# Performance work log

Measured on AMD Instinct MI355X. Metric: run time of the kernel, lower is better.

Reference implementation:

```python
import jax, jax.numpy as jnp
import numpy as np

B, C, O, H, W = 4, 256, 256, 64, 64
KH = KW = 3
KK = KH * KW
PAD = 1  # stride=1, padding=1 -> output spatial == input spatial


def setup_inputs() -> dict:
    key = jax.random.key(0)
    k0, k1, k2, k3 = jax.random.split(key, 4)
    x = jax.random.normal(k0, (B, C, H, W), jnp.float32)
    # offset-predicting conv: small weights -> realistic sub-pixel offsets
    w_off = jax.random.normal(k1, (3 * KK, C, KH, KW), jnp.float32) * 0.01
    b_off = jnp.zeros((3 * KK,), jnp.float32)
    w_def = jax.random.normal(k2, (O, C, KH, KW), jnp.float32) * (1.0 / np.sqrt(C * KK))
    b_def = jax.random.normal(k3, (O,), jnp.float32) * 0.01
    return {"x": x, "w_off": w_off, "b_off": b_off, "w_def": w_def, "b_def": b_def}


def _conv2d(x, w, b):
    y = jax.lax.conv_general_dilated(
        x, w, window_strides=(1, 1), padding=((PAD, PAD), (PAD, PAD)),
        dimension_numbers=("NCHW", "OIHW", "NCHW"))
    return y + b[None, :, None, None]


def _deform_conv2d(x, offsets, mask, w, b):
    # torchvision modulated DeformConv2d, stride=1, pad=1, dilation=1.
    Bx, Cx, Hx, Wx = x.shape
    Ox = w.shape[0]
    # offsets: [B, 2*KK, H, W] with channel 2k = dy, 2k+1 = dx for tap k
    off = offsets.reshape(Bx, KK, 2, Hx, Wx)
    ky, kx = jnp.meshgrid(jnp.arange(KH), jnp.arange(KW), indexing="ij")
    ky = ky.reshape(KK)
    kx = kx.reshape(KK)
    base_y = (ky[:, None, None] - PAD + jnp.arange(Hx)[None, :, None]).astype(x.dtype)  # [KK,H,1]
    base_x = (kx[:, None, None] - PAD + jnp.arange(Wx)[None, None, :]).astype(x.dtype)  # [KK,1,W]
    sy = off[:, :, 0] + base_y  # [B,KK,H,W] sample rows
    sx = off[:, :, 1] + base_x  # [B,KK,H,W] sample cols

    y0 = jnp.floor(sy)
    x0 = jnp.floor(sx)
    ty = sy - y0  # fractional weights (grad flows to offsets through these)
    tx = sx - x0

    x_flat = x.reshape(Bx, Cx, Hx * Wx)
    val = jnp.zeros((Bx, Cx, KK, Hx, Wx), x.dtype)
    for dy in (0, 1):  # 4 bilinear corners (fixed small loop)
        for dx in (0, 1):
            yi = y0.astype(jnp.int32) + dy
            xi = x0.astype(jnp.int32) + dx
            wgt = (ty if dy else 1.0 - ty) * (tx if dx else 1.0 - tx)
            valid = (yi >= 0) & (yi < Hx) & (xi >= 0) & (xi < Wx)  # zero outside
            idx = (jnp.clip(yi, 0, Hx - 1) * Wx + jnp.clip(xi, 0, Wx - 1)).reshape(Bx, 1, -1)
            g = jnp.take_along_axis(x_flat, idx, axis=2).reshape(Bx, Cx, KK, Hx, Wx)
            val = val + g * jnp.where(valid, wgt, 0.0)[:, None]

    val = val * mask.reshape(Bx, 1, KK, Hx, Wx)  # modulation
    out = jnp.einsum("bckhw,ock->bohw", val, w.reshape(Ox, Cx, KK))
    return out + b[None, :, None, None]


def reference(x, w_off, b_off, w_def, b_def):
    pred = _conv2d(x, w_off, b_off)            # [B, 3*KK, H, W]
    offsets = pred[:, : 2 * KK]                # [B, 2*KK, H, W]
    mask = jax.nn.sigmoid(pred[:, 2 * KK:])    # [B, KK, H, W]
    return _deform_conv2d(x, offsets, mask, w_def, b_def)
```

## Files before the change

kernel.cpp:

```cpp
#include <hip/hip_runtime.h>

#define BB 4
#define CCH 256
#define OCH 256
#define HH 64
#define WW 64
#define HWSZ 4096

typedef __bf16 bf16_t;
typedef bf16_t bf16x8 __attribute__((ext_vector_type(8)));
typedef bf16_t bf16x2_t __attribute__((ext_vector_type(2)));
typedef float f32x4 __attribute__((ext_vector_type(4)));

__device__ __forceinline__ unsigned int packbf(float a, float b) {
    bf16x2_t p;
    p.x = (__bf16)a;
    p.y = (__bf16)b;
    return __builtin_bit_cast(unsigned int, p);
}
__device__ __forceinline__ float blo(unsigned int u) { return __uint_as_float(u << 16); }
__device__ __forceinline__ float bhi(unsigned int u) { return __uint_as_float(u & 0xFFFF0000u); }

__device__ __forceinline__ void block_sync() {
    asm volatile("s_waitcnt lgkmcnt(0)" ::: "memory");
    __builtin_amdgcn_s_barrier();
    __builtin_amdgcn_sched_barrier(0);
}

__global__ __launch_bounds__(256) void k_prep(const float* __restrict__ x,
                                              const float* __restrict__ w_off,
                                              const float* __restrict__ w_def,
                                              ushort* __restrict__ xT,
                                              ushort* __restrict__ w1F,
                                              ushort* __restrict__ w2F,
                                              float* __restrict__ P) {
    int bid = blockIdx.x;
    if (bid < 256) {
        int b = bid >> 6;
        int h = bid & 63;
        int tid = threadIdx.x;
        int wv = tid >> 6;
        int lane = tid & 63;

        __shared__ unsigned int buf[64][130];

        const float* xp = x + ((size_t)b * CCH + wv * 64) * HWSZ + h * WW + lane;
#pragma unroll 8
        for (int i = 0; i < 32; ++i) {
            float a = xp[(size_t)(2 * i) * HWSZ];
            float c = xp[(size_t)(2 * i + 1) * HWSZ];
            buf[lane][wv * 32 + i] = packbf(a, c);
        }
        __syncthreads();

        ushort* dst = xT + ((size_t)(b * 64 + h) * 64) * 256;
#pragma unroll
        for (int r = 0; r < 16; ++r) {
            int idx = tid + r * 256;
            int w = idx >> 6;
            int q = idx & 63;
            uint2 v = *(const uint2*)&buf[w][2 * q];
            *(uint2*)(dst + (size_t)w * 256 + q * 4) = v;
        }
        return;
    }

    int i = (bid - 256) * 256 + threadIdx.x;
    if (i < 73728) {
        int j = i & 7;
        int o = (i >> 3) & 31;
        int cSub = (i >> 8) & 31;
        int k = i >> 13;
        float v = 0.0f;
        if (o < 27) v = w_off[((size_t)o * CCH + cSub * 8 + j) * 9 + k];
        w1F[i] = (ushort)(packbf(v, 0.f) & 0xFFFFu);
        return;
    }
    i -= 73728;
    if (i < 589824) {
        int j = i & 7;
        int o = (i >> 3) & 255;
        int cg = (i >> 11) & 31;
        int k = i >> 16;
        float v = w_def[(size_t)o * 2304 + (cg * 8 + j) * 9 + k];
        w2F[i] = (ushort)(packbf(v, 0.f) & 0xFFFFu);
        return;
    }
    i -= 589824;
    if (i < 110592) {
        ((float4*)P)[i] = make_float4(0.f, 0.f, 0.f, 0.f);
    }
}

__global__ __launch_bounds__(512) void k_pred4(const ushort* __restrict__ xT,
                                               const ushort* __restrict__ w1F,
                                               float* __restrict__ P) {
    int bid = blockIdx.x;
    int L = (bid & 7) * 64 + (bid >> 3);
    int cs = L & 3;
    int hg = (L >> 2) & 31;
    int b  = L >> 7;
    int tid = threadIdx.x;
    int lane = tid & 63;
    int wv   = tid >> 6;
    int l16  = lane & 15;
    int lq   = lane >> 4;
    int spx  = tid >> 3;
    int cl   = tid & 7;

    __shared__ ushort b_lds[2][8][8][16][8];

    const ushort* xTb = xT + (size_t)b * HWSZ * 256 + cs * 64 + cl * 8;
    const bf16x8* w1v = (const bf16x8*)w1F;

    f32x4 acc[2];
    acc[0] = (f32x4){0.f, 0.f, 0.f, 0.f};
    acc[1] = (f32x4){0.f, 0.f, 0.f, 0.f};

    auto stageLoad = [&](int k, int tpx) -> uint4 {
        int row = hg * 2 + (tpx >> 6);
        int col = tpx & 63;
        int ys = row + k / 3 - 1;
        int xs = col + k % 3 - 1;
        bool ok = (ys >= 0 && ys < HH && xs >= 0 && xs < WW);
        uint4 v = make_uint4(0u, 0u, 0u, 0u);
        if (ok) v = *(const uint4*)(xTb + (size_t)(ys * WW + xs) * 256);
        return v;
    };
    auto stageWrite = [&](uint4 v, int buf, int tpx) {
        *(uint4*)&b_lds[buf][cl][tpx >> 4][(tpx & 15) ^ cl][0] = v;
    };

    {
        uint4 v0 = stageLoad(0, spx);
        uint4 v1 = stageLoad(0, spx + 64);
        stageWrite(v0, 0, spx);
        stageWrite(v1, 0, spx + 64);
    }
    __syncthreads();

    for (int t = 0; t < 9; ++t) {
        int cur = t & 1;
        uint4 n0, n1;
        if (t < 8) {
            n0 = stageLoad(t + 1, spx);
            n1 = stageLoad(t + 1, spx + 64);
        }
        bf16x8 a00 = w1v[(size_t)(t * 32 + cs * 8 + 0 * 4 + lq) * 32 + 0 * 16 + l16];
        bf16x8 a01 = w1v[(size_t)(t * 32 + cs * 8 + 0 * 4 + lq) * 32 + 1 * 16 + l16];
        bf16x8 a10 = w1v[(size_t)(t * 32 + cs * 8 + 1 * 4 + lq) * 32 + 0 * 16 + l16];
        bf16x8 a11 = w1v[(size_t)(t * 32 + cs * 8 + 1 * 4 + lq) * 32 + 1 * 16 + l16];
        bf16x8 b0 = *(const bf16x8*)&b_lds[cur][0 * 4 + lq][wv][l16 ^ (0 * 4 + lq)][0];
        bf16x8 b1 = *(const bf16x8*)&b_lds[cur][1 * 4 + lq][wv][l16 ^ (1 * 4 + lq)][0];
        acc[0] = __builtin_amdgcn_mfma_f32_16x16x32_bf16(a00, b0, acc[0], 0, 0, 0);
        acc[1] = __builtin_amdgcn_mfma_f32_16x16x32_bf16(a01, b0, acc[1], 0, 0, 0);
        acc[0] = __builtin_amdgcn_mfma_f32_16x16x32_bf16(a10, b1, acc[0], 0, 0, 0);
        acc[1] = __builtin_amdgcn_mfma_f32_16x16x32_bf16(a11, b1, acc[1], 0, 0, 0);
        if (t < 8) {
            stageWrite(n0, cur ^ 1, spx);
            stageWrite(n1, cur ^ 1, spx + 64);
        }
        __syncthreads();
    }

    int prow = hg * 2 + (wv >> 2);
    int pcol = (wv & 3) * 16 + l16;
#pragma unroll
    for (int mf = 0; mf < 2; ++mf) {
#pragma unroll
        for (int r = 0; r < 4; ++r) {
            int o = mf * 16 + lq * 4 + r;
            if (o < 27) {
                atomicAdd(&P[((size_t)b * 27 + o) * HWSZ + prow * WW + pcol],
                          acc[mf][r]);
            }
        }
    }
}

__global__ __launch_bounds__(512, 4) void k_deform15(const ushort* __restrict__ xT,
                                                     const float* __restrict__ P,
                                                     const float* __restrict__ b_off,
                                                     const ushort* __restrict__ w2F,
                                                     const float* __restrict__ b_def,
                                                     float* __restrict__ out) {
    int bid = blockIdx.x;
    int L = (bid & 7) * 64 + (bid >> 3);
    int ph = L & 1;
    int h  = (L >> 1) & 63;
    int b  = L >> 7;
    int px0 = ph * 32;
    int tid = threadIdx.x;
    int lane = tid & 63;
    int wv   = tid >> 6;
    int l16  = lane & 15;
    int lq   = lane >> 4;
    int pxs  = tid >> 4;
    int cl   = tid & 15;

    __shared__ ushort b_lds[2][16][2][16][8];

    const char* xTc = (const char*)xT + (size_t)b * HWSZ * 512 + cl * 16;
    const bf16x8* w2b = (const bf16x8*)w2F + wv * 32 + l16;

    uint4* wdst0 = (uint4*)&b_lds[0][cl][pxs >> 4][(pxs & 15) ^ cl][0];
    uint4* wdst1 = (uint4*)&b_lds[1][cl][pxs >> 4][(pxs & 15) ^ cl][0];

    f32x4 acc[2][2];
#pragma unroll
    for (int mf = 0; mf < 2; ++mf)
#pragma unroll
        for (int nt = 0; nt < 2; ++nt) acc[mf][nt] = (f32x4){0.f, 0.f, 0.f, 0.f};

    const float* Pb = P + (size_t)b * 27 * HWSZ + h * WW + px0 + pxs;

    float pOy, pOx, pMr, bOy, bOx, bMr;
    float wgt[4];
    const char* aptr[4];

    auto loadP = [&](int k) {
        pOy = Pb[(size_t)(2 * k) * HWSZ];
        pOx = Pb[(size_t)(2 * k + 1) * HWSZ];
        pMr = Pb[(size_t)(18 + k) * HWSZ];
        bOy = b_off[2 * k];
        bOx = b_off[2 * k + 1];
        bMr = b_off[18 + k];
    };
    auto calcDesc = [&](int k) {
        float offy = pOy + bOy;
        float offx = pOx + bOx;
        float m = 1.0f / (1.0f + expf(-(pMr + bMr)));
        float sy = offy + (float)(h + k / 3 - 1);
        float sx = offx + (float)(px0 + pxs + k % 3 - 1);
        float y0f = floorf(sy), x0f = floorf(sx);
        float ty = sy - y0f, tx = sx - x0f;
        int y0 = (int)y0f, x0 = (int)x0f;
#pragma unroll
        for (int dy = 0; dy < 2; ++dy) {
#pragma unroll
            for (int dx = 0; dx < 2; ++dx) {
                int yi = y0 + dy, xi = x0 + dx;
                bool ok = (yi >= 0 && yi < HH && xi >= 0 && xi < WW);
                float wg = (dy ? ty : 1.0f - ty) * (dx ? tx : 1.0f - tx) * m;
                wgt[dy * 2 + dx]  = ok ? wg : 0.0f;
                aptr[dy * 2 + dx] = xTc + (size_t)(ok ? (yi * WW + xi) : 0) * 512;
            }
        }
    };

    uint4 gbA[4], gbB[4];
    float wgtA[4], wgtB[4];
    bf16x8 aA[2][4], aB[2][4];

    auto issueGatherTo = [&](uint4 (&gb)[4], float (&wg)[4], int off) {
#pragma unroll
        for (int c = 0; c < 4; ++c) gb[c] = *(const uint4*)(aptr[c] + off);
#pragma unroll
        for (int c = 0; c < 4; ++c) wg[c] = wgt[c];
    };
    auto combineFrom = [&](const uint4 (&g)[4], const float (&w)[4]) -> uint4 {
        uint4 r;
        {
            float lo = w[0]*blo(g[0].x) + w[1]*blo(g[1].x) + w[2]*blo(g[2].x) + w[3]*blo(g[3].x);
            float hi = w[0]*bhi(g[0].x) + w[1]*bhi(g[1].x) + w[2]*bhi(g[2].x) + w[3]*bhi(g[3].x);
            r.x = packbf(lo, hi);
        }
        {
            float lo = w[0]*blo(g[0].y) + w[1]*blo(g[1].y) + w[2]*blo(g[2].y) + w[3]*blo(g[3].y);
            float hi = w[0]*bhi(g[0].y) + w[1]*bhi(g[1].y) + w[2]*bhi(g[2].y) + w[3]*bhi(g[3].y);
            r.y = packbf(lo, hi);
        }
        {
            float lo = w[0]*blo(g[0].z) + w[1]*blo(g[1].z) + w[2]*blo(g[2].z) + w[3]*blo(g[3].z);
            float hi = w[0]*bhi(g[0].z) + w[1]*bhi(g[1].z) + w[2]*bhi(g[2].z) + w[3]*bhi(g[3].z);
            r.z = packbf(lo, hi);
        }
        {
            float lo = w[0]*blo(g[0].w) + w[1]*blo(g[1].w) + w[2]*blo(g[2].w) + w[3]*blo(g[3].w);
            float hi = w[0]*bhi(g[0].w) + w[1]*bhi(g[1].w) + w[2]*bhi(g[2].w) + w[3]*bhi(g[3].w);
            r.w = packbf(lo, hi);
        }
        return r;
    };
    auto loadATo = [&](bf16x8 (&a)[2][4], int t) {
        size_t base = ((size_t)((t >> 1) * 32 + (t & 1) * 16) + lq) * 256;
#pragma unroll
        for (int g = 0; g < 4; ++g)
#pragma unroll
            for (int mf = 0; mf < 2; ++mf)
                a[mf][g] = w2b[base + (size_t)g * 1024 + mf * 16];
    };

#define MFMA_BODY(BUF, AREG)                                                        \
    do {                                                                            \
        bf16x8 bfr[4][2];                                                           \
        _Pragma("unroll")                                                           \
        for (int g = 0; g < 4; ++g) {                                               \
            int kg = g * 4 + lq;                                                    \
            _Pragma("unroll")                                                       \
            for (int nt = 0; nt < 2; ++nt)                                          \
                bfr[g][nt] = *(const bf16x8*)&b_lds[BUF][kg][nt][l16 ^ kg][0];      \
        }                                                                           \
        _Pragma("unroll")                                                           \
        for (int g = 0; g < 4; ++g)                                                 \
            _Pragma("unroll")                                                       \
            for (int mf = 0; mf < 2; ++mf)                                          \
                _Pragma("unroll")                                                   \
                for (int nt = 0; nt < 2; ++nt)                                      \
                    acc[mf][nt] = __builtin_amdgcn_mfma_f32_16x16x32_bf16(          \
                        AREG[mf][g], bfr[g][nt], acc[mf][nt], 0, 0, 0);             \
    } while (0)

    loadP(0);
    calcDesc(0);
    issueGatherTo(gbA, wgtA, 0);
    issueGatherTo(gbB, wgtB, 256);
    loadP(1);
    loadATo(aA, 0);
    *wdst0 = combineFrom(gbA, wgtA);
    __syncthreads();

    for (int tp = 0; tp < 9; ++tp) {
        if (tp < 8) {
            calcDesc(tp + 1);
            issueGatherTo(gbA, wgtA, 0);
        }
        loadATo(aB, 2 * tp + 1);
        MFMA_BODY(0, aA);
        *wdst1 = combineFrom(gbB, wgtB);
        __syncthreads();

        if (tp < 8) {
            issueGatherTo(gbB, wgtB, 256);
            if (tp < 7) loadP(tp + 2);
            loadATo(aA, 2 * tp + 2);
        }
        MFMA_BODY(1, aB);
        if (tp < 8) {
            *wdst0 = combineFrom(gbA, wgtA);
        }
        __syncthreads();
    }
#undef MFMA_BODY

#pragma unroll
    for (int mf = 0; mf < 2; ++mf) {
#pragma unroll
        for (int nt = 0; nt < 2; ++nt) {
#pragma unroll
            for (int r = 0; r < 4; ++r) {
                int o = wv * 32 + mf * 16 + lq * 4 + r;
                out[((size_t)b * OCH + o) * HWSZ + h * WW + px0 + nt * 16 + l16] =
                    acc[mf][nt][r] + b_def[o];
            }
        }
    }
}

extern "C" void kernel_launch(void* const* d_in, const int* in_sizes, int n_in,
                              void* d_out, int out_size, void* d_ws, size_t ws_size,
                              hipStream_t stream) {
    const float* x     = (const float*)d_in[0];
    const float* w_off = (const float*)d_in[1];
    const float* b_off = (const float*)d_in[2];
    const float* w_def = (const float*)d_in[3];
    const float* b_def = (const float*)d_in[4];
    float* out = (float*)d_out;

    float*  P   = (float*)d_ws;
    ushort* w1F = (ushort*)(P + (size_t)BB * 27 * HWSZ);
    ushort* w2F = w1F + 73728;
    ushort* xT  = w2F + 589824;

    hipLaunchKernelGGL(k_prep, dim3(3280), dim3(256), 0, stream,
                       x, w_off, w_def, xT, w1F, w2F, P);
    hipLaunchKernelGGL(k_pred4, dim3(512), dim3(512), 0, stream, xT, w1F, P);
    hipLaunchKernelGGL(k_deform15, dim3(512), dim3(512), 0, stream,
                       xT, P, b_off, w2F, b_def, out);
}
```

Before: 76.58 us.

## Restructure deform pipeline to process whole tap per stage with double-buffered LDS

```diff
diff --git a/kernel.cpp b/kernel.cpp
--- a/kernel.cpp
+++ b/kernel.cpp
@@ -20,12 +20,6 @@
 }
 __device__ __forceinline__ float blo(unsigned int u) { return __uint_as_float(u << 16); }
 __device__ __forceinline__ float bhi(unsigned int u) { return __uint_as_float(u & 0xFFFF0000u); }
-
-__device__ __forceinline__ void block_sync() {
-    asm volatile("s_waitcnt lgkmcnt(0)" ::: "memory");
-    __builtin_amdgcn_s_barrier();
-    __builtin_amdgcn_sched_barrier(0);
-}
 
 __global__ __launch_bounds__(256) void k_prep(const float* __restrict__ x,
                                               const float* __restrict__ w_off,
@@ -178,7 +172,7 @@
     }
 }
 
-__global__ __launch_bounds__(512, 4) void k_deform15(const ushort* __restrict__ xT,
+__global__ __launch_bounds__(512, 4) void k_deform16(const ushort* __restrict__ xT,
                                                      const float* __restrict__ P,
                                                      const float* __restrict__ b_off,
                                                      const ushort* __restrict__ w2F,
@@ -198,13 +192,15 @@
     int pxs  = tid >> 4;
     int cl   = tid & 15;
 
-    __shared__ ushort b_lds[2][16][2][16][8];
+    __shared__ ushort b_lds[2][2][16][2][16][8];
 
     const char* xTc = (const char*)xT + (size_t)b * HWSZ * 512 + cl * 16;
     const bf16x8* w2b = (const bf16x8*)w2F + wv * 32 + l16;
 
-    uint4* wdst0 = (uint4*)&b_lds[0][cl][pxs >> 4][(pxs & 15) ^ cl][0];
-    uint4* wdst1 = (uint4*)&b_lds[1][cl][pxs >> 4][(pxs & 15) ^ cl][0];
+    uint4* wdst00 = (uint4*)&b_lds[0][0][cl][pxs >> 4][(pxs & 15) ^ cl][0];
+    uint4* wdst01 = (uint4*)&b_lds[0][1][cl][pxs >> 4][(pxs & 15) ^ cl][0];
+    uint4* wdst10 = (uint4*)&b_lds[1][0][cl][pxs >> 4][(pxs & 15) ^ cl][0];
+    uint4* wdst11 = (uint4*)&b_lds[1][1][cl][pxs >> 4][(pxs & 15) ^ cl][0];
 
     f32x4 acc[2][2];
 #pragma unroll
@@ -249,41 +245,38 @@
     };
 
     uint4 gbA[4], gbB[4];
-    float wgtA[4], wgtB[4];
     bf16x8 aA[2][4], aB[2][4];
 
-    auto issueGatherTo = [&](uint4 (&gb)[4], float (&wg)[4], int off) {
+    auto issueGatherTo = [&](uint4 (&gb)[4], int off) {
 #pragma unroll
         for (int c = 0; c < 4; ++c) gb[c] = *(const uint4*)(aptr[c] + off);
-#pragma unroll
-        for (int c = 0; c < 4; ++c) wg[c] = wgt[c];
-    };
-    auto combineFrom = [&](const uint4 (&g)[4], const float (&w)[4]) -> uint4 {
+    };
+    auto combineFrom = [&](const uint4 (&g)[4]) -> uint4 {
         uint4 r;
         {
-            float lo = w[0]*blo(g[0].x) + w[1]*blo(g[1].x) + w[2]*blo(g[2].x) + w[3]*blo(g[3].x);
-            float hi = w[0]*bhi(g[0].x) + w[1]*bhi(g[1].x) + w[2]*bhi(g[2].x) + w[3]*bhi(g[3].x);
+            float lo = wgt[0]*blo(g[0].x) + wgt[1]*blo(g[1].x) + wgt[2]*blo(g[2].x) + wgt[3]*blo(g[3].x);
+            float hi = wgt[0]*bhi(g[0].x) + wgt[1]*bhi(g[1].x) + wgt[2]*bhi(g[2].x) + wgt[3]*bhi(g[3].x);
             r.x = packbf(lo, hi);
         }
         {
-            float lo = w[0]*blo(g[0].y) + w[1]*blo(g[1].y) + w[2]*blo(g[2].y) + w[3]*blo(g[3].y);
-            float hi = w[0]*bhi(g[0].y) + w[1]*bhi(g[1].y) + w[2]*bhi(g[2].y) + w[3]*bhi(g[3].y);
+            float lo = wgt[0]*blo(g[0].y) + wgt[1]*blo(g[1].y) + wgt[2]*blo(g[2].y) + wgt[3]*blo(g[3].y);
+            float hi = wgt[0]*bhi(g[0].y) + wgt[1]*bhi(g[1].y) + wgt[2]*bhi(g[2].y) + wgt[3]*bhi(g[3].y);
             r.y = packbf(lo, hi);
         }
         {
-            float lo = w[0]*blo(g[0].z) + w[1]*blo(g[1].z) + w[2]*blo(g[2].z) + w[3]*blo(g[3].z);
-            float hi = w[0]*bhi(g[0].z) + w[1]*bhi(g[1].z) + w[2]*bhi(g[2].z) + w[3]*bhi(g[3].z);
+            float lo = wgt[0]*blo(g[0].z) + wgt[1]*blo(g[1].z) + wgt[2]*blo(g[2].z) + wgt[3]*blo(g[3].z);
+            float hi = wgt[0]*bhi(g[0].z) + wgt[1]*bhi(g[1].z) + wgt[2]*bhi(g[2].z) + wgt[3]*bhi(g[3].z);
             r.z = packbf(lo, hi);
         }
         {
-            float lo = w[0]*blo(g[0].w) + w[1]*blo(g[1].w) + w[2]*blo(g[2].w) + w[3]*blo(g[3].w);
-            float hi = w[0]*bhi(g[0].w) + w[1]*bhi(g[1].w) + w[2]*bhi(g[2].w) + w[3]*bhi(g[3].w);
+            float lo = wgt[0]*blo(g[0].w) + wgt[1]*blo(g[1].w) + wgt[2]*blo(g[2].w) + wgt[3]*blo(g[3].w);
+            float hi = wgt[0]*bhi(g[0].w) + wgt[1]*bhi(g[1].w) + wgt[2]*bhi(g[2].w) + wgt[3]*bhi(g[3].w);
             r.w = packbf(lo, hi);
         }
         return r;
     };
-    auto loadATo = [&](bf16x8 (&a)[2][4], int t) {
-        size_t base = ((size_t)((t >> 1) * 32 + (t & 1) * 16) + lq) * 256;
+    auto loadATo = [&](bf16x8 (&a)[2][4], int t, int s) {
+        size_t base = ((size_t)(t * 32 + s * 16) + lq) * 256;
 #pragma unroll
         for (int g = 0; g < 4; ++g)
 #pragma unroll
@@ -291,7 +284,7 @@
                 a[mf][g] = w2b[base + (size_t)g * 1024 + mf * 16];
     };
 
-#define MFMA_BODY(BUF, AREG)                                                        \
+#define MFMA_SUB(BUF, SUB, AREG)                                                    \
     do {                                                                            \
         bf16x8 bfr[4][2];                                                           \
         _Pragma("unroll")                                                           \
@@ -299,7 +292,7 @@
             int kg = g * 4 + lq;                                                    \
             _Pragma("unroll")                                                       \
             for (int nt = 0; nt < 2; ++nt)                                          \
-                bfr[g][nt] = *(const bf16x8*)&b_lds[BUF][kg][nt][l16 ^ kg][0];      \
+                bfr[g][nt] = *(const bf16x8*)&b_lds[BUF][SUB][kg][nt][l16 ^ kg][0]; \
         }                                                                           \
         _Pragma("unroll")                                                           \
         for (int g = 0; g < 4; ++g)                                                 \
@@ -313,35 +306,48 @@
 
     loadP(0);
     calcDesc(0);
-    issueGatherTo(gbA, wgtA, 0);
-    issueGatherTo(gbB, wgtB, 256);
+    issueGatherTo(gbA, 0);
+    issueGatherTo(gbB, 256);
     loadP(1);
-    loadATo(aA, 0);
-    *wdst0 = combineFrom(gbA, wgtA);
+    loadATo(aA, 0, 0);
+    loadATo(aB, 0, 1);
+    *wdst00 = combineFrom(gbA);
+    *wdst01 = combineFrom(gbB);
     __syncthreads();
 
-    for (int tp = 0; tp < 9; ++tp) {
-        if (tp < 8) {
-            calcDesc(tp + 1);
-            issueGatherTo(gbA, wgtA, 0);
-        }
-        loadATo(aB, 2 * tp + 1);
-        MFMA_BODY(0, aA);
-        *wdst1 = combineFrom(gbB, wgtB);
-        __syncthreads();
-
-        if (tp < 8) {
-            issueGatherTo(gbB, wgtB, 256);
-            if (tp < 7) loadP(tp + 2);
-            loadATo(aA, 2 * tp + 2);
-        }
-        MFMA_BODY(1, aB);
-        if (tp < 8) {
-            *wdst0 = combineFrom(gbA, wgtA);
-        }
-        __syncthreads();
-    }
-#undef MFMA_BODY
+    for (int tp = 0; tp < 4; ++tp) {
+        {
+            int t = 2 * tp;
+            calcDesc(t + 1);
+            issueGatherTo(gbA, 0);
+            issueGatherTo(gbB, 256);
+            if (t < 7) loadP(t + 2);
+            MFMA_SUB(0, 0, aA);
+            loadATo(aA, t + 1, 0);
+            MFMA_SUB(0, 1, aB);
+            loadATo(aB, t + 1, 1);
+            *wdst10 = combineFrom(gbA);
+            *wdst11 = combineFrom(gbB);
+            __syncthreads();
+        }
+        {
+            int t = 2 * tp + 1;
+            calcDesc(t + 1);
+            issueGatherTo(gbA, 0);
+            issueGatherTo(gbB, 256);
+            if (t < 7) loadP(t + 2);
+            MFMA_SUB(1, 0, aA);
+            loadATo(aA, t + 1, 0);
+            MFMA_SUB(1, 1, aB);
+            loadATo(aB, t + 1, 1);
+            *wdst00 = combineFrom(gbA);
+            *wdst01 = combineFrom(gbB);
+            __syncthreads();
+        }
+    }
+    MFMA_SUB(0, 0, aA);
+    MFMA_SUB(0, 1, aB);
+#undef MFMA_SUB
 
 #pragma unroll
     for (int mf = 0; mf < 2; ++mf) {
@@ -375,6 +381,6 @@
     hipLaunchKernelGGL(k_prep, dim3(3280), dim3(256), 0, stream,
                        x, w_off, w_def, xT, w1F, w2F, P);
     hipLaunchKernelGGL(k_pred4, dim3(512), dim3(512), 0, stream, xT, w1F, P);
-    hipLaunchKernelGGL(k_deform15, dim3(512), dim3(512), 0, stream,
+    hipLaunchKernelGGL(k_deform16, dim3(512), dim3(512), 0, stream,
                        xT, P, b_off, w2F, b_def, out);
 }
```

Result: slower. 82.84 us (+8.2%).

## Split deform kernel output channels across two blocks to double grid size

Applied to the files above, without the earlier changes.

```diff
diff --git a/kernel.cpp b/kernel.cpp
--- a/kernel.cpp
+++ b/kernel.cpp
@@ -20,12 +20,6 @@
 }
 __device__ __forceinline__ float blo(unsigned int u) { return __uint_as_float(u << 16); }
 __device__ __forceinline__ float bhi(unsigned int u) { return __uint_as_float(u & 0xFFFF0000u); }
-
-__device__ __forceinline__ void block_sync() {
-    asm volatile("s_waitcnt lgkmcnt(0)" ::: "memory");
-    __builtin_amdgcn_s_barrier();
-    __builtin_amdgcn_sched_barrier(0);
-}
 
 __global__ __launch_bounds__(256) void k_prep(const float* __restrict__ x,
                                               const float* __restrict__ w_off,
@@ -178,17 +172,18 @@
     }
 }
 
-__global__ __launch_bounds__(512, 4) void k_deform15(const ushort* __restrict__ xT,
+__global__ __launch_bounds__(512, 4) void k_deform17(const ushort* __restrict__ xT,
                                                      const float* __restrict__ P,
                                                      const float* __restrict__ b_off,
                                                      const ushort* __restrict__ w2F,
                                                      const float* __restrict__ b_def,
                                                      float* __restrict__ out) {
     int bid = blockIdx.x;
-    int L = (bid & 7) * 64 + (bid >> 3);
-    int ph = L & 1;
-    int h  = (L >> 1) & 63;
-    int b  = L >> 7;
+    int L = (bid & 7) * 128 + (bid >> 3);
+    int os = L & 1;
+    int ph = (L >> 1) & 1;
+    int h  = (L >> 2) & 63;
+    int b  = L >> 8;
     int px0 = ph * 32;
     int tid = threadIdx.x;
     int lane = tid & 63;
@@ -201,16 +196,14 @@
     __shared__ ushort b_lds[2][16][2][16][8];
 
     const char* xTc = (const char*)xT + (size_t)b * HWSZ * 512 + cl * 16;
-    const bf16x8* w2b = (const bf16x8*)w2F + wv * 32 + l16;
+    const bf16x8* w2b = (const bf16x8*)w2F + os * 128 + wv * 16 + l16;
 
     uint4* wdst0 = (uint4*)&b_lds[0][cl][pxs >> 4][(pxs & 15) ^ cl][0];
     uint4* wdst1 = (uint4*)&b_lds[1][cl][pxs >> 4][(pxs & 15) ^ cl][0];
 
-    f32x4 acc[2][2];
-#pragma unroll
-    for (int mf = 0; mf < 2; ++mf)
-#pragma unroll
-        for (int nt = 0; nt < 2; ++nt) acc[mf][nt] = (f32x4){0.f, 0.f, 0.f, 0.f};
+    f32x4 acc[2];
+    acc[0] = (f32x4){0.f, 0.f, 0.f, 0.f};
+    acc[1] = (f32x4){0.f, 0.f, 0.f, 0.f};
 
     const float* Pb = P + (size_t)b * 27 * HWSZ + h * WW + px0 + pxs;
 
@@ -250,7 +243,7 @@
 
     uint4 gbA[4], gbB[4];
     float wgtA[4], wgtB[4];
-    bf16x8 aA[2][4], aB[2][4];
+    bf16x8 aA[4], aB[4];
 
     auto issueGatherTo = [&](uint4 (&gb)[4], float (&wg)[4], int off) {
 #pragma unroll
@@ -282,13 +275,11 @@
         }
         return r;
     };
-    auto loadATo = [&](bf16x8 (&a)[2][4], int t) {
+    auto loadATo = [&](bf16x8 (&a)[4], int t) {
         size_t base = ((size_t)((t >> 1) * 32 + (t & 1) * 16) + lq) * 256;
 #pragma unroll
         for (int g = 0; g < 4; ++g)
-#pragma unroll
-            for (int mf = 0; mf < 2; ++mf)
-                a[mf][g] = w2b[base + (size_t)g * 1024 + mf * 16];
+            a[g] = w2b[base + (size_t)g * 1024];
     };
 
 #define MFMA_BODY(BUF, AREG)                                                        \
@@ -304,11 +295,9 @@
         _Pragma("unroll")                                                           \
         for (int g = 0; g < 4; ++g)                                                 \
             _Pragma("unroll")                                                       \
-            for (int mf = 0; mf < 2; ++mf)                                          \
-                _Pragma("unroll")                                                   \
-                for (int nt = 0; nt < 2; ++nt)                                      \
-                    acc[mf][nt] = __builtin_amdgcn_mfma_f32_16x16x32_bf16(          \
-                        AREG[mf][g], bfr[g][nt], acc[mf][nt], 0, 0, 0);             \
+            for (int nt = 0; nt < 2; ++nt)                                          \
+                acc[nt] = __builtin_amdgcn_mfma_f32_16x16x32_bf16(                  \
+                    AREG[g], bfr[g][nt], acc[nt], 0, 0, 0);                         \
     } while (0)
 
     loadP(0);
@@ -344,15 +333,12 @@
 #undef MFMA_BODY
 
 #pragma unroll
-    for (int mf = 0; mf < 2; ++mf) {
-#pragma unroll
-        for (int nt = 0; nt < 2; ++nt) {
-#pragma unroll
-            for (int r = 0; r < 4; ++r) {
-                int o = wv * 32 + mf * 16 + lq * 4 + r;
-                out[((size_t)b * OCH + o) * HWSZ + h * WW + px0 + nt * 16 + l16] =
-                    acc[mf][nt][r] + b_def[o];
-            }
+    for (int nt = 0; nt < 2; ++nt) {
+#pragma unroll
+        for (int r = 0; r < 4; ++r) {
+            int o = os * 128 + wv * 16 + lq * 4 + r;
+            out[((size_t)b * OCH + o) * HWSZ + h * WW + px0 + nt * 16 + l16] =
+                acc[nt][r] + b_def[o];
         }
     }
 }
@@ -375,6 +361,6 @@
     hipLaunchKernelGGL(k_prep, dim3(3280), dim3(256), 0, stream,
                        x, w_off, w_def, xT, w1F, w2F, P);
     hipLaunchKernelGGL(k_pred4, dim3(512), dim3(512), 0, stream, xT, w1F, P);
-    hipLaunchKernelGGL(k_deform15, dim3(512), dim3(512), 0, stream,
+    hipLaunchKernelGGL(k_deform17, dim3(1024), dim3(512), 0, stream,
                        xT, P, b_off, w2F, b_def, out);
 }
```

Result: no change. 77.05 us, median of 2 (+0.6%).
